# Kernel tuning notes

Measured on AMD Instinct MI355X. Metric: run time of the kernel, lower is better.

## Reference

```python
import jax, jax.numpy as jnp
import numpy as np
from jax import lax

STRIDES = (8, 16, 32, 64, 128)
LEVEL_HW = ((100, 128), (50, 64), (25, 32), (13, 16), (7, 8))
NUM_CLASSES = 80
PRE_NMS_THRESH = 0.05
PRE_NMS_TOPK = 1000
NMS_THRESH = 0.6
MAX_DET = 100
CLS_OFFSET = 1.0e4  # > max image coordinate, separates classes for joint NMS


def setup_inputs() -> dict:
    key = jax.random.key(0)
    B = 16
    ks = jax.random.split(key, 3 * len(LEVEL_HW))
    inp = {}
    i = 0
    for lvl, (h, w) in enumerate(LEVEL_HW):
        # shift logits down so sigmoid scores are mostly below the 0.05 candidate
        # threshold (realistic detection sparsity)
        inp[f"logits_p{lvl + 3}"] = jax.random.normal(ks[i], (B, NUM_CLASSES, h, w), jnp.float32) - 4.0; i += 1
        inp[f"bbox_p{lvl + 3}"] = jax.random.uniform(ks[i], (B, 4, h, w), jnp.float32, minval=0.0, maxval=64.0); i += 1
        inp[f"ctr_p{lvl + 3}"] = jax.random.normal(ks[i], (B, 1, h, w), jnp.float32); i += 1
    inp["im_info"] = jnp.tile(jnp.array([[800.0, 1024.0]], jnp.float32), (B, 1))
    return inp


def _locations(h, w, stride):
    # FCOSLocation: center of each stride cell -> [HW, 2] as (x, y)
    sx = jnp.arange(w, dtype=jnp.float32) * stride + stride // 2
    sy = jnp.arange(h, dtype=jnp.float32) * stride + stride // 2
    yy, xx = jnp.meshgrid(sy, sx, indexing="ij")
    return jnp.stack([xx.reshape(-1), yy.reshape(-1)], axis=-1)


def _nms_single(boxes, scores, classes):
    # boxes [K,4], scores [K] (descending), classes [K] int
    off = classes.astype(jnp.float32)[:, None] * CLS_OFFSET
    nb = boxes + off  # class-offset trick -> per-class NMS in one pass
    areas = jnp.maximum(nb[:, 2] - nb[:, 0], 0.0) * jnp.maximum(nb[:, 3] - nb[:, 1], 0.0)

    def body(sc, _):
        i = jnp.argmax(sc)
        s = sc[i]
        bi = nb[i]
        xx1 = jnp.maximum(bi[0], nb[:, 0])
        yy1 = jnp.maximum(bi[1], nb[:, 1])
        xx2 = jnp.minimum(bi[2], nb[:, 2])
        yy2 = jnp.minimum(bi[3], nb[:, 3])
        inter = jnp.maximum(xx2 - xx1, 0.0) * jnp.maximum(yy2 - yy1, 0.0)
        iou = inter / (areas[i] + areas - inter + 1e-9)
        sc2 = jnp.where(iou >= NMS_THRESH, -jnp.inf, sc).at[i].set(-jnp.inf)
        return sc2, (i, s > 0.0)

    _, (idxs, valid) = lax.scan(body, scores, None, length=MAX_DET)
    det = jnp.concatenate(
        [boxes[idxs], scores[idxs][:, None], classes[idxs].astype(jnp.float32)[:, None]],
        axis=-1,
    )  # [MAX_DET, 6] = x1,y1,x2,y2,score,class
    return jnp.where(valid[:, None], det, 0.0)


def _forward(logits_p3, bbox_p3, ctr_p3, logits_p4, bbox_p4, ctr_p4,
             logits_p5, bbox_p5, ctr_p5, logits_p6, bbox_p6, ctr_p6,
             logits_p7, bbox_p7, ctr_p7, im_info):
    levels = [(logits_p3, bbox_p3, ctr_p3), (logits_p4, bbox_p4, ctr_p4),
              (logits_p5, bbox_p5, ctr_p5), (logits_p6, bbox_p6, ctr_p6),
              (logits_p7, bbox_p7, ctr_p7)]
    scores_l, boxes_l = [], []
    for (lg, rg, ct), stride in zip(levels, STRIDES):
        B, C, H, W = lg.shape
        cls = jax.nn.sigmoid(lg).transpose(0, 2, 3, 1).reshape(B, H * W, C)
        cen = jax.nn.sigmoid(ct).transpose(0, 2, 3, 1).reshape(B, H * W, 1)
        # candidate threshold on raw class prob, then modulate by centerness
        comb = jnp.where(cls > PRE_NMS_THRESH, cls * cen, 0.0)
        locs = _locations(H, W, stride)  # [HW, 2]
        reg = rg.transpose(0, 2, 3, 1).reshape(B, H * W, 4)  # (l, t, r, b)
        bx = jnp.stack([locs[None, :, 0] - reg[..., 0],
                        locs[None, :, 1] - reg[..., 1],
                        locs[None, :, 0] + reg[..., 2],
                        locs[None, :, 1] + reg[..., 3]], axis=-1)
        scores_l.append(comb)
        boxes_l.append(bx)
    scores = jnp.concatenate(scores_l, axis=1)  # [B, N, C]
    boxes = jnp.concatenate(boxes_l, axis=1)    # [B, N, 4]
    B, N, C = scores.shape
    vals, idx = lax.top_k(scores.reshape(B, N * C), PRE_NMS_TOPK)  # [B, K]
    loc = idx // C
    cls_id = idx % C
    cand = jnp.take_along_axis(boxes, loc[..., None], axis=1)  # [B, K, 4]
    h = im_info[:, 0:1]
    w = im_info[:, 1:2]
    x1 = jnp.clip(cand[..., 0], 0.0, w - 1.0)
    y1 = jnp.clip(cand[..., 1], 0.0, h - 1.0)
    x2 = jnp.clip(cand[..., 2], 0.0, w - 1.0)
    y2 = jnp.clip(cand[..., 3], 0.0, h - 1.0)
    cand = jnp.stack([x1, y1, x2, y2], axis=-1)
    sc = jnp.where(vals > 0.0, jnp.sqrt(jnp.maximum(vals, 0.0) + 1e-12), 0.0)
    return jax.vmap(_nms_single)(cand, sc, cls_id)  # [B, MAX_DET, 6]


def reference(logits_p3, bbox_p3, ctr_p3, logits_p4, bbox_p4, ctr_p4,
              logits_p5, bbox_p5, ctr_p5, logits_p6, bbox_p6, ctr_p6,
              logits_p7, bbox_p7, ctr_p7, im_info):
    return _forward(logits_p3, bbox_p3, ctr_p3, logits_p4, bbox_p4, ctr_p4,
                    logits_p5, bbox_p5, ctr_p5, logits_p6, bbox_p6, ctr_p6,
                    logits_p7, bbox_p7, ctr_p7, im_info)
```

## Files before the change

### kernel.cpp

```cpp
#include <hip/hip_runtime.h>
#include <math.h>

#pragma clang fp contract(off)

#define NB 16
#define NC 80
#define NTOT 17064
#define TOPK 1000
#define NBINS 8192
#define CAP 4096
#define MAXDET 100
#define NREP 4
#define CNTSTRIDE 64
#define CHUNK 128
#define G1 128
#define NSEG 512
#define SEGW 1024

struct Ptrs {
    const float* lg[5];
    const float* bb[5];
    const float* ct[5];
};

__device__ __forceinline__ void level_of(int n, int& l, int& hw, int& W,
                                         int& stride, int& half, int& HW) {
    if (n < 12800)      { l = 0; hw = n;         W = 128; stride = 8;   half = 4;  HW = 12800; }
    else if (n < 16000) { l = 1; hw = n - 12800; W = 64;  stride = 16;  half = 8;  HW = 3200;  }
    else if (n < 16800) { l = 2; hw = n - 16000; W = 32;  stride = 32;  half = 16; HW = 800;   }
    else if (n < 17008) { l = 3; hw = n - 16800; W = 16;  stride = 64;  half = 32; HW = 208;   }
    else                { l = 4; hw = n - 17008; W = 8;   stride = 128; half = 64; HW = 56;    }
}

__device__ __forceinline__ float fast_sig(float x) {
    float e = __expf(-x);
    return __builtin_amdgcn_rcpf(1.0f + e);
}

template<int HW4, int NF4, int LVOFF, bool WRITE>
__device__ __forceinline__ void sweep_level(const float* lgb, const float* ctb,
        int tid, int lane, int bx, int gx, unsigned* lh32,
        unsigned long long* segp, unsigned& cur, unsigned long long ltmask) {
    for (int i0 = bx * 256; i0 < NF4; i0 += gx * 256) {
        int i = i0 + tid;
        bool f0 = false, f1 = false, f2 = false, f3 = false;
        unsigned long long k0 = 0, k1 = 0, k2 = 0, k3 = 0;
        if (i < NF4) {
            int c   = i / HW4;
            int hwf = i - c * HW4;
            float4 v  = *(const float4*)(lgb + c * (HW4 * 4) + hwf * 4);
            if (v.x > -2.95f || v.y > -2.95f || v.z > -2.95f || v.w > -2.95f) {
                float4 cv = *(const float4*)(ctb + hwf * 4);
                int nbase = LVOFF + hwf * 4;
#define DO_J(J, X, CT, F, K)                                                  \
                if ((X) > -2.95f) {                \
                    float cls = fast_sig(X);                                  \
                    if (cls > 0.04999f) {                                     \
                        bool in = true;                                       \
                        if (cls < 0.05001f)      \
                            in = (1.0f / (1.0f + expf(-(X)))) > 0.05f;        \
                        if (in) {                                             \
                            float cen = fast_sig(CT);                         \
                            float comb = cls * cen;                           \
                            unsigned bits = __float_as_uint(comb);            \
                            unsigned cb = (bits > 32u) ? bits - 32u : 0u;     \
                            unsigned bin = cb >> 19;                          \
                            atomicAdd(&lh32[bin >> 1],                        \
                                      (bin & 1u) ? 0x10000u : 1u);            \
                            if (WRITE) {                                      \
                                unsigned idx = (unsigned)((nbase + (J)) * NC + c);\
                                K = ((unsigned long long)bits << 32) |        \
                                    (0xFFFFFFFFu - idx);                      \
                                F = true;                                     \
                            }                                                 \
                        }                                                     \
                    }                                                         \
                }
                DO_J(0, v.x, cv.x, f0, k0)
                DO_J(1, v.y, cv.y, f1, k1)
                DO_J(2, v.z, cv.z, f2, k2)
                DO_J(3, v.w, cv.w, f3, k3)
#undef DO_J
            }
        }
        if (WRITE) {
            unsigned long long m0 = __ballot(f0), m1 = __ballot(f1);
            unsigned long long m2 = __ballot(f2), m3 = __ballot(f3);
            if ((m0 | m1 | m2 | m3) == 0ULL) continue;
            unsigned t0 = (unsigned)__popcll(m0), t1 = (unsigned)__popcll(m1);
            unsigned t2 = (unsigned)__popcll(m2), t3 = (unsigned)__popcll(m3);
            if (f0) { unsigned pos = cur + (unsigned)__popcll(m0 & ltmask);                if (pos < SEGW) segp[pos] = k0; }
            if (f1) { unsigned pos = cur + t0 + (unsigned)__popcll(m1 & ltmask);           if (pos < SEGW) segp[pos] = k1; }
            if (f2) { unsigned pos = cur + t0 + t1 + (unsigned)__popcll(m2 & ltmask);      if (pos < SEGW) segp[pos] = k2; }
            if (f3) { unsigned pos = cur + t0 + t1 + t2 + (unsigned)__popcll(m3 & ltmask); if (pos < SEGW) segp[pos] = k3; }
            cur += t0 + t1 + t2 + t3;
        }
    }
}

template<bool WRITE>
__global__ void __launch_bounds__(256) k_score1(Ptrs p, unsigned* hist,
                                                unsigned* segcnt,
                                                unsigned long long* segbuf) {
    __shared__ unsigned lh32[NBINS / 2];
    int b = blockIdx.y, tid = threadIdx.x, bx = blockIdx.x, gx = gridDim.x;
    int lane = tid & 63, wv = tid >> 6;
    unsigned long long ltmask = (1ULL << lane) - 1ULL;
    for (int i = tid; i < NBINS / 2; i += 256) lh32[i] = 0;
    __syncthreads();

    unsigned long long* segp = WRITE
        ? segbuf + (((size_t)b * G1 + bx) * 4 + wv) * SEGW : nullptr;
    unsigned cur = 0;

    sweep_level<3200, 256000,     0, WRITE>(p.lg[0] + (size_t)b * NC * 12800, p.ct[0] + (size_t)b * 12800, tid, lane, bx, gx, lh32, segp, cur, ltmask);
    sweep_level< 800,  64000, 12800, WRITE>(p.lg[1] + (size_t)b * NC * 3200,  p.ct[1] + (size_t)b * 3200,  tid, lane, bx, gx, lh32, segp, cur, ltmask);
    sweep_level< 200,  16000, 16000, WRITE>(p.lg[2] + (size_t)b * NC * 800,   p.ct[2] + (size_t)b * 800,   tid, lane, bx, gx, lh32, segp, cur, ltmask);
    sweep_level<  52,   4160, 16800, WRITE>(p.lg[3] + (size_t)b * NC * 208,   p.ct[3] + (size_t)b * 208,   tid, lane, bx, gx, lh32, segp, cur, ltmask);
    sweep_level<  14,   1120, 17008, WRITE>(p.lg[4] + (size_t)b * NC * 56,    p.ct[4] + (size_t)b * 56,    tid, lane, bx, gx, lh32, segp, cur, ltmask);

    if (WRITE && lane == 0)
        segcnt[(size_t)b * NSEG + bx * 4 + wv] = (cur < SEGW) ? cur : SEGW;

    __syncthreads();
    unsigned* h = hist + ((size_t)(bx & (NREP - 1)) * NB + b) * NBINS;
    for (int i = tid; i < NBINS; i += 256) {
        unsigned v = (lh32[i >> 1] >> ((i & 1) * 16)) & 0xFFFFu;
        if (v) atomicAdd(&h[i], v);
    }
}

__global__ void __launch_bounds__(256) k_thresh(const unsigned* hist, unsigned* T) {
    __shared__ unsigned hl[NBINS];
    __shared__ unsigned wtot[4];
    __shared__ int Tf;
    int b = blockIdx.x, tid = threadIdx.x, lane = tid & 63, wv = tid >> 6;
    if (tid == 0) Tf = 0;
    for (int i = tid; i < NBINS; i += 256) {
        unsigned s = 0;
        for (int r = 0; r < NREP; ++r)
            s += hist[((size_t)r * NB + b) * NBINS + i];
        hl[i] = s;
    }
    __syncthreads();
    int base = tid * 32;
    unsigned mysum = 0;
#pragma unroll
    for (int i = 0; i < 32; ++i) mysum += hl[base + i];
    unsigned incl = mysum;
#pragma unroll
    for (int off = 1; off < 64; off <<= 1) {
        unsigned v = __shfl_down(incl, off);
        if (lane + off < 64) incl += v;
    }
    if (lane == 0) wtot[wv] = incl;
    __syncthreads();
    unsigned above = 0;
    for (int w = wv + 1; w < 4; ++w) above += wtot[w];
    unsigned sufincl = incl + above;
    unsigned excl = sufincl - mysum;
    if (excl < TOPK && sufincl >= TOPK) {
        unsigned running = excl;
        for (int bin = base + 31; bin >= base; --bin) {
            running += hl[bin];
            if (running >= TOPK) { Tf = bin; break; }
        }
    }
    __syncthreads();
    if (tid == 0) T[b] = (unsigned)Tf;
}

__global__ void __launch_bounds__(256) k_filter(Ptrs p, const unsigned* T,
                                                const unsigned* segcnt,
                                                const unsigned long long* segbuf,
                                                unsigned* cnt2, unsigned long long* sel) {
    int b = blockIdx.y, tid = threadIdx.x, lane = tid & 63;
    unsigned Tb = T[b];
    unsigned Tshift = Tb << 19;
    unsigned fmin = (Tshift >= 32u) ? Tshift - 32u : 0u;
    unsigned long long ltmask = (1ULL << lane) - 1ULL;
    unsigned* cntb = cnt2 + (size_t)b * CNTSTRIDE;
    unsigned long long* selb = sel + (size_t)b * CAP;

    for (int sg = blockIdx.x * 16; sg < blockIdx.x * 16 + 16; ++sg) {
        unsigned sc = segcnt[(size_t)b * NSEG + sg];
        const unsigned long long* src = segbuf + ((size_t)b * NSEG + sg) * SEGW;
        for (int i = tid; i < (int)sc; i += 256) {
            unsigned long long e = src[i];
            bool f = false;
            unsigned long long key = 0;
            if ((unsigned)(e >> 32) >= fmin) {
                unsigned idx = 0xFFFFFFFFu - (unsigned)(e & 0xFFFFFFFFu);
                int n = idx / NC, c = idx - n * NC;
                int l, hw, W, stride, half, HW;
                level_of(n, l, hw, W, stride, half, HW);
                float x  = p.lg[l][(size_t)b * NC * HW + (size_t)c * HW + hw];
                float ct = p.ct[l][(size_t)b * HW + hw];
                float cls = 1.0f / (1.0f + expf(-x));
                float cen = 1.0f / (1.0f + expf(-ct));
                unsigned be = __float_as_uint(cls * cen);
                if ((be >> 19) >= Tb) {
                    key = ((unsigned long long)be << 32) | (e & 0xFFFFFFFFULL);
                    f = true;
                }
            }
            unsigned long long mk = __ballot(f);
            if (mk) {
                unsigned nw = (unsigned)__popcll(mk);
                int basep = 0;
                if (lane == 0) basep = (int)atomicAdd(cntb, nw);
                basep = __shfl(basep, 0);
                if (f) {
                    int pos = basep + (int)__popcll(mk & ltmask);
                    if (pos < CAP) selb[pos] = key;
                }
            }
        }
    }
}

template<int HW4, int NF4, int LVOFF>
__device__ __forceinline__ void compact_level(const float* lgb, const float* ctb,
        int tid, int lane, int bx, int gx, unsigned Tb, float xpre,
        unsigned* cntb, unsigned long long* selb, unsigned long long ltmask) {
    for (int i0 = bx * 256; i0 < NF4; i0 += gx * 256) {
        int i = i0 + tid;
        bool f0 = false, f1 = false, f2 = false, f3 = false;
        unsigned long long k0 = 0, k1 = 0, k2 = 0, k3 = 0;
        if (i < NF4) {
            int c   = i / HW4;
            int hwf = i - c * HW4;
            float4 v = *(const float4*)(lgb + c * (HW4 * 4) + hwf * 4);
            if (v.x > xpre || v.y > xpre || v.z > xpre || v.w > xpre) {
                float4 cv = *(const float4*)(ctb + hwf * 4);
                int nbase = LVOFF + hwf * 4;
#define DO_J(J, X, CT, F, K)                                                  \
                if ((X) > xpre) {                                             \
                    float cls = 1.0f / (1.0f + expf(-(X)));                   \
                    if (cls > 0.05f) {                                        \
                        float cen = 1.0f / (1.0f + expf(-(CT)));              \
                        float comb = cls * cen;                               \
                        unsigned bits = __float_as_uint(comb);                \
                        if ((bits >> 19) >= Tb) {                             \
                            unsigned idx = (unsigned)((nbase + (J)) * NC + c);\
                            K = ((unsigned long long)bits << 32) |            \
                                (0xFFFFFFFFu - idx);                          \
                            F = true;                                         \
                        }                                                     \
                    }                                                         \
                }
                DO_J(0, v.x, cv.x, f0, k0)
                DO_J(1, v.y, cv.y, f1, k1)
                DO_J(2, v.z, cv.z, f2, k2)
                DO_J(3, v.w, cv.w, f3, k3)
#undef DO_J
            }
        }
        unsigned long long m0 = __ballot(f0), m1 = __ballot(f1);
        unsigned long long m2 = __ballot(f2), m3 = __ballot(f3);
        if ((m0 | m1 | m2 | m3) == 0ULL) continue;
        unsigned t0 = (unsigned)__popcll(m0), t1 = (unsigned)__popcll(m1);
        unsigned t2 = (unsigned)__popcll(m2), t3 = (unsigned)__popcll(m3);
        unsigned total = t0 + t1 + t2 + t3;
        int basep = 0;
        if (lane == 0) basep = (int)atomicAdd(cntb, total);
        basep = __shfl(basep, 0);
        if (f0) { int pos = basep + (int)__popcll(m0 & ltmask);                       if (pos < CAP) selb[pos] = k0; }
        if (f1) { int pos = basep + (int)t0 + (int)__popcll(m1 & ltmask);             if (pos < CAP) selb[pos] = k1; }
        if (f2) { int pos = basep + (int)(t0 + t1) + (int)__popcll(m2 & ltmask);      if (pos < CAP) selb[pos] = k2; }
        if (f3) { int pos = basep + (int)(t0 + t1 + t2) + (int)__popcll(m3 & ltmask); if (pos < CAP) selb[pos] = k3; }
    }
}

__global__ void __launch_bounds__(256) k_compactB(Ptrs p, const unsigned* T,
                                                  unsigned* cnt2, unsigned long long* sel) {
    int b = blockIdx.y, tid = threadIdx.x, lane = tid & 63;
    int bx = blockIdx.x, gx = gridDim.x;
    unsigned Tb = T[b];
    float mthr = __uint_as_float(Tb << 19);
    float xpre = -2.95f;
    if (mthr > 1e-37f && mthr < 1.0f) {
        float lm = logf(mthr / (1.0f - mthr)) - 0.01f;
        if (lm > xpre) xpre = lm;
    }
    unsigned long long ltmask = (1ULL << lane) - 1ULL;
    unsigned* cntb = cnt2 + (size_t)b * CNTSTRIDE;
    unsigned long long* selb = sel + (size_t)b * CAP;
    compact_level<3200, 256000,     0>(p.lg[0] + (size_t)b * NC * 12800, p.ct[0] + (size_t)b * 12800, tid, lane, bx, gx, Tb, xpre, cntb, selb, ltmask);
    compact_level< 800,  64000, 12800>(p.lg[1] + (size_t)b * NC * 3200,  p.ct[1] + (size_t)b * 3200,  tid, lane, bx, gx, Tb, xpre, cntb, selb, ltmask);
    compact_level< 200,  16000, 16000>(p.lg[2] + (size_t)b * NC * 800,   p.ct[2] + (size_t)b * 800,   tid, lane, bx, gx, Tb, xpre, cntb, selb, ltmask);
    compact_level<  52,   4160, 16800>(p.lg[3] + (size_t)b * NC * 208,   p.ct[3] + (size_t)b * 208,   tid, lane, bx, gx, Tb, xpre, cntb, selb, ltmask);
    compact_level<  14,   1120, 17008>(p.lg[4] + (size_t)b * NC * 56,    p.ct[4] + (size_t)b * 56,    tid, lane, bx, gx, Tb, xpre, cntb, selb, ltmask);
}

__global__ void __launch_bounds__(256) k_rankdec(Ptrs p, const unsigned* cnt,
                                                 const unsigned long long* sel,
                                                 const float* im_info, float* cand) {
    __shared__ __align__(16) unsigned long long keys[CAP];
    int b = blockIdx.y, tid = threadIdx.x;
    unsigned M = cnt[(size_t)b * CNTSTRIDE];
    if (M > CAP) M = CAP;
    int s0 = blockIdx.x * 256;
    if (s0 >= (int)M) return;
    int Mpad = (int)((M + 1u) & ~1u);
    for (int i = tid; i < Mpad; i += 256)
        keys[i] = (i < (int)M) ? sel[(size_t)b * CAP + i] : 0ULL;
    __syncthreads();

    int s = s0 + tid;
    if (s >= (int)M) return;
    unsigned long long k = keys[s];
    int rank = 0;
    for (int j = 0; j < Mpad; j += 2) {
        ulonglong2 kk = *(const ulonglong2*)&keys[j];
        rank += (kk.x > k) ? 1 : 0;
        rank += (kk.y > k) ? 1 : 0;
    }
    if (rank >= TOPK) return;

    float Him = im_info[b * 2 + 0], Wim = im_info[b * 2 + 1];
    float xmax = Wim - 1.0f, ymax = Him - 1.0f;
    unsigned sb = (unsigned)(k >> 32);
    unsigned idx = 0xFFFFFFFFu - (unsigned)(k & 0xFFFFFFFFu);
    float val = __uint_as_float(sb);
    int n = idx / NC, c = idx - n * NC;
    int l, hw, W, stride, half, HW;
    level_of(n, l, hw, W, stride, half, HW);
    int wx = hw % W, hy = hw / W;
    float locx = (float)(wx * stride + half);
    float locy = (float)(hy * stride + half);
    const float* bb = p.bb[l] + (size_t)b * 4 * HW + hw;
    float r0 = bb[0], r1 = bb[(size_t)HW], r2 = bb[(size_t)2 * HW], r3 = bb[(size_t)3 * HW];
    float x1 = locx - r0, y1 = locy - r1, x2 = locx + r2, y2 = locy + r3;
    x1 = fminf(fmaxf(x1, 0.f), xmax);
    y1 = fminf(fmaxf(y1, 0.f), ymax);
    x2 = fminf(fmaxf(x2, 0.f), xmax);
    y2 = fminf(fmaxf(y2, 0.f), ymax);
    float scv = sqrtf(val + 1e-12f);
    float off = (float)c * 10000.0f;
    float a0 = x1 + off, a1 = y1 + off, a2 = x2 + off, a3 = y2 + off;
    float area = fmaxf(a2 - a0, 0.f) * fmaxf(a3 - a1, 0.f);
    float* dst = cand + ((size_t)b * TOPK + rank) * 12;
    *(float4*)(dst + 0) = make_float4(x1, y1, x2, y2);
    *(float4*)(dst + 4) = make_float4(a0, a1, a2, a3);
    *(float4*)(dst + 8) = make_float4(area, scv, (float)c, 0.f);
}

__global__ void __launch_bounds__(64) k_nms(const unsigned* cnt, const float* cand,
                                            float* out) {
    __shared__ float4 s_ob[CHUNK], s_nb[CHUNK], s_ms[CHUNK];
    int b = blockIdx.x, lane = threadIdx.x;
    unsigned M = cnt[(size_t)b * CNTSTRIDE];
    if (M > CAP) M = CAP;
    int ncand = (int)M < TOPK ? (int)M : TOPK;
    const float* src = cand + (size_t)b * TOPK * 12;
    float* ob = out + (size_t)b * MAXDET * 6;

    int na = 0;
    float4 a0b = make_float4(0.f, 0.f, 0.f, 0.f);
    float4 a1b = make_float4(0.f, 0.f, 0.f, 0.f);
    float a0a = 0.f, a1a = 0.f;

    for (int base = 0; base < ncand && na < MAXDET; base += CHUNK) {
        int cn = ncand - base; if (cn > CHUNK) cn = CHUNK;
        for (int cidx = lane; cidx < cn; cidx += 64) {
            const float* s = src + (size_t)(base + cidx) * 12;
            s_ob[cidx] = *(const float4*)(s + 0);
            s_nb[cidx] = *(const float4*)(s + 4);
            s_ms[cidx] = *(const float4*)(s + 8);
        }
        __syncthreads();
        for (int r = 0; r < cn && na < MAXDET; ++r) {
            float4 cb = s_nb[r];
            float ca = s_ms[r].x;
            bool sup = false;
            if (lane < na) {
                float xx1 = fmaxf(a0b.x, cb.x);
                float yy1 = fmaxf(a0b.y, cb.y);
                float xx2 = fminf(a0b.z, cb.z);
                float yy2 = fminf(a0b.w, cb.w);
                float inter = fmaxf(xx2 - xx1, 0.f) * fmaxf(yy2 - yy1, 0.f);
                float iou = inter / (((a0a + ca) - inter) + 1e-9f);
                sup = (iou >= 0.6f);
            }
            if (lane + 64 < na) {
                float xx1 = fmaxf(a1b.x, cb.x);
                float yy1 = fmaxf(a1b.y, cb.y);
                float xx2 = fminf(a1b.z, cb.z);
                float yy2 = fminf(a1b.w, cb.w);
                float inter = fmaxf(xx2 - xx1, 0.f) * fmaxf(yy2 - yy1, 0.f);
                float iou = inter / (((a1a + ca) - inter) + 1e-9f);
                sup |= (iou >= 0.6f);
            }
            if (__ballot(sup) == 0ULL) {
                if (lane == (na & 63)) {
                    if (na < 64) { a0b = cb; a0a = ca; }
                    else         { a1b = cb; a1a = ca; }
                }
                if (lane == 0) {
                    float4 o4 = s_ob[r]; float4 m4 = s_ms[r];
                    ob[na * 6 + 0] = o4.x; ob[na * 6 + 1] = o4.y;
                    ob[na * 6 + 2] = o4.z; ob[na * 6 + 3] = o4.w;
                    ob[na * 6 + 4] = m4.y; ob[na * 6 + 5] = m4.z;
                }
                ++na;
            }
        }
        __syncthreads();
    }
    for (int q = na * 6 + lane; q < MAXDET * 6; q += 64)
        ob[q] = 0.f;
}

extern "C" void kernel_launch(void* const* d_in, const int* in_sizes, int n_in,
                              void* d_out, int out_size, void* d_ws, size_t ws_size,
                              hipStream_t stream) {
    Ptrs p;
    for (int l = 0; l < 5; ++l) {
        p.lg[l] = (const float*)d_in[3 * l + 0];
        p.bb[l] = (const float*)d_in[3 * l + 1];
        p.ct[l] = (const float*)d_in[3 * l + 2];
    }
    const float* im_info = (const float*)d_in[15];
    float* out = (float*)d_out;

    unsigned char* w = (unsigned char*)d_ws;
    unsigned* hist          = (unsigned*)(w);
    unsigned* cnt2          = (unsigned*)(w + 2097152);
    unsigned* T             = (unsigned*)(w + 2101248);
    unsigned long long* sel = (unsigned long long*)(w + 2101504);
    float* cand             = (float*)(w + 2625792);
    unsigned* segcnt        = (unsigned*)(w + 3393792);
    unsigned long long* segbuf = (unsigned long long*)(w + 3426560);
    const bool big = ws_size >= (size_t)70535424;

    hipMemsetAsync(w, 0, 2101504, stream);

    if (big) {
        k_score1<true ><<<dim3(G1, NB), 256, 0, stream>>>(p, hist, segcnt, segbuf);
        k_thresh<<<NB, 256, 0, stream>>>(hist, T);
        k_filter<<<dim3(NSEG / 16, NB), 256, 0, stream>>>(p, T, segcnt, segbuf, cnt2, sel);
    } else {
        k_score1<false><<<dim3(G1, NB), 256, 0, stream>>>(p, hist, nullptr, nullptr);
        k_thresh<<<NB, 256, 0, stream>>>(hist, T);
        k_compactB<<<dim3(128, NB), 256, 0, stream>>>(p, T, cnt2, sel);
    }
    k_rankdec<<<dim3(16, NB), 256, 0, stream>>>(p, cnt2, sel, im_info, cand);
    k_nms<<<NB, 64, 0, stream>>>(cnt2, cand, out);
}
```

Baseline: 257.2 us.

## Prefilter candidates at fixed score floor and build histogram from compacted segments

```diff
diff --git a/kernel.cpp b/kernel.cpp
--- a/kernel.cpp
+++ b/kernel.cpp
@@ -15,7 +15,7 @@
 #define CHUNK 128
 #define G1 128
 #define NSEG 512
-#define SEGW 1024
+#define SEGW 512
 
 struct Ptrs {
     const float* lg[5];
@@ -37,9 +37,9 @@
     return __builtin_amdgcn_rcpf(1.0f + e);
 }
 
-template<int HW4, int NF4, int LVOFF, bool WRITE>
-__device__ __forceinline__ void sweep_level(const float* lgb, const float* ctb,
-        int tid, int lane, int bx, int gx, unsigned* lh32,
+template<int HW4, int NF4, int LVOFF>
+__device__ __forceinline__ void scan_level(const float* lgb, const float* ctb,
+        int tid, int lane, int bx, int gx, unsigned FB_LO,
         unsigned long long* segp, unsigned& cur, unsigned long long ltmask) {
     for (int i0 = bx * 256; i0 < NF4; i0 += gx * 256) {
         int i = i0 + tid;
@@ -48,32 +48,20 @@
         if (i < NF4) {
             int c   = i / HW4;
             int hwf = i - c * HW4;
-            float4 v  = *(const float4*)(lgb + c * (HW4 * 4) + hwf * 4);
-            if (v.x > -2.95f || v.y > -2.95f || v.z > -2.95f || v.w > -2.95f) {
+            float4 v = *(const float4*)(lgb + c * (HW4 * 4) + hwf * 4);
+            if (v.x > -2.47f || v.y > -2.47f || v.z > -2.47f || v.w > -2.47f) {
                 float4 cv = *(const float4*)(ctb + hwf * 4);
                 int nbase = LVOFF + hwf * 4;
 #define DO_J(J, X, CT, F, K)                                                  \
-                if ((X) > -2.95f) {                \
+                if ((X) > -2.47f) {                                           \
                     float cls = fast_sig(X);                                  \
-                    if (cls > 0.04999f) {                                     \
-                        bool in = true;                                       \
-                        if (cls < 0.05001f)      \
-                            in = (1.0f / (1.0f + expf(-(X)))) > 0.05f;        \
-                        if (in) {                                             \
-                            float cen = fast_sig(CT);                         \
-                            float comb = cls * cen;                           \
-                            unsigned bits = __float_as_uint(comb);            \
-                            unsigned cb = (bits > 32u) ? bits - 32u : 0u;     \
-                            unsigned bin = cb >> 19;                          \
-                            atomicAdd(&lh32[bin >> 1],                        \
-                                      (bin & 1u) ? 0x10000u : 1u);            \
-                            if (WRITE) {                                      \
-                                unsigned idx = (unsigned)((nbase + (J)) * NC + c);\
-                                K = ((unsigned long long)bits << 32) |        \
-                                    (0xFFFFFFFFu - idx);                      \
-                                F = true;                                     \
-                            }                                                 \
-                        }                                                     \
+                    float cen = fast_sig(CT);                                 \
+                    unsigned bits = __float_as_uint(cls * cen);               \
+                    if (bits >= FB_LO) {                                      \
+                        unsigned idx = (unsigned)((nbase + (J)) * NC + c);    \
+                        K = ((unsigned long long)bits << 32) |                \
+                            (0xFFFFFFFFu - idx);                              \
+                        F = true;                                             \
                     }                                                         \
                 }
                 DO_J(0, v.x, cv.x, f0, k0)
@@ -83,70 +71,131 @@
 #undef DO_J
             }
         }
-        if (WRITE) {
-            unsigned long long m0 = __ballot(f0), m1 = __ballot(f1);
-            unsigned long long m2 = __ballot(f2), m3 = __ballot(f3);
-            if ((m0 | m1 | m2 | m3) == 0ULL) continue;
-            unsigned t0 = (unsigned)__popcll(m0), t1 = (unsigned)__popcll(m1);
-            unsigned t2 = (unsigned)__popcll(m2), t3 = (unsigned)__popcll(m3);
-            if (f0) { unsigned pos = cur + (unsigned)__popcll(m0 & ltmask);                if (pos < SEGW) segp[pos] = k0; }
-            if (f1) { unsigned pos = cur + t0 + (unsigned)__popcll(m1 & ltmask);           if (pos < SEGW) segp[pos] = k1; }
-            if (f2) { unsigned pos = cur + t0 + t1 + (unsigned)__popcll(m2 & ltmask);      if (pos < SEGW) segp[pos] = k2; }
-            if (f3) { unsigned pos = cur + t0 + t1 + t2 + (unsigned)__popcll(m3 & ltmask); if (pos < SEGW) segp[pos] = k3; }
-            cur += t0 + t1 + t2 + t3;
-        }
-    }
-}
-
-template<bool WRITE>
-__global__ void __launch_bounds__(256) k_score1(Ptrs p, unsigned* hist,
-                                                unsigned* segcnt,
-                                                unsigned long long* segbuf) {
-    __shared__ unsigned lh32[NBINS / 2];
+        unsigned long long m0 = __ballot(f0), m1 = __ballot(f1);
+        unsigned long long m2 = __ballot(f2), m3 = __ballot(f3);
+        if ((m0 | m1 | m2 | m3) == 0ULL) continue;
+        unsigned t0 = (unsigned)__popcll(m0), t1 = (unsigned)__popcll(m1);
+        unsigned t2 = (unsigned)__popcll(m2), t3 = (unsigned)__popcll(m3);
+        if (f0) { unsigned pos = cur + (unsigned)__popcll(m0 & ltmask);                if (pos < SEGW) segp[pos] = k0; }
+        if (f1) { unsigned pos = cur + t0 + (unsigned)__popcll(m1 & ltmask);           if (pos < SEGW) segp[pos] = k1; }
+        if (f2) { unsigned pos = cur + t0 + t1 + (unsigned)__popcll(m2 & ltmask);      if (pos < SEGW) segp[pos] = k2; }
+        if (f3) { unsigned pos = cur + t0 + t1 + t2 + (unsigned)__popcll(m3 & ltmask); if (pos < SEGW) segp[pos] = k3; }
+        cur += t0 + t1 + t2 + t3;
+    }
+}
+
+__global__ void __launch_bounds__(256) k_scoreF(Ptrs p, unsigned* segcnt,
+                                                unsigned long long* segbuf,
+                                                unsigned* cnt2) {
     int b = blockIdx.y, tid = threadIdx.x, bx = blockIdx.x, gx = gridDim.x;
     int lane = tid & 63, wv = tid >> 6;
+    if (bx == 0 && tid == 0) cnt2[(size_t)b * CNTSTRIDE] = 0;
     unsigned long long ltmask = (1ULL << lane) - 1ULL;
-    for (int i = tid; i < NBINS / 2; i += 256) lh32[i] = 0;
-    __syncthreads();
-
-    unsigned long long* segp = WRITE
-        ? segbuf + (((size_t)b * G1 + bx) * 4 + wv) * SEGW : nullptr;
+    unsigned FB_LO = __float_as_uint(0.08f) - 64u;
+    unsigned long long* segp = segbuf + (((size_t)b * G1 + bx) * 4 + wv) * SEGW;
     unsigned cur = 0;
 
-    sweep_level<3200, 256000,     0, WRITE>(p.lg[0] + (size_t)b * NC * 12800, p.ct[0] + (size_t)b * 12800, tid, lane, bx, gx, lh32, segp, cur, ltmask);
-    sweep_level< 800,  64000, 12800, WRITE>(p.lg[1] + (size_t)b * NC * 3200,  p.ct[1] + (size_t)b * 3200,  tid, lane, bx, gx, lh32, segp, cur, ltmask);
-    sweep_level< 200,  16000, 16000, WRITE>(p.lg[2] + (size_t)b * NC * 800,   p.ct[2] + (size_t)b * 800,   tid, lane, bx, gx, lh32, segp, cur, ltmask);
-    sweep_level<  52,   4160, 16800, WRITE>(p.lg[3] + (size_t)b * NC * 208,   p.ct[3] + (size_t)b * 208,   tid, lane, bx, gx, lh32, segp, cur, ltmask);
-    sweep_level<  14,   1120, 17008, WRITE>(p.lg[4] + (size_t)b * NC * 56,    p.ct[4] + (size_t)b * 56,    tid, lane, bx, gx, lh32, segp, cur, ltmask);
-
-    if (WRITE && lane == 0)
-        segcnt[(size_t)b * NSEG + bx * 4 + wv] = (cur < SEGW) ? cur : SEGW;
-
-    __syncthreads();
-    unsigned* h = hist + ((size_t)(bx & (NREP - 1)) * NB + b) * NBINS;
-    for (int i = tid; i < NBINS; i += 256) {
-        unsigned v = (lh32[i >> 1] >> ((i & 1) * 16)) & 0xFFFFu;
-        if (v) atomicAdd(&h[i], v);
-    }
-}
-
-__global__ void __launch_bounds__(256) k_thresh(const unsigned* hist, unsigned* T) {
-    __shared__ unsigned hl[NBINS];
-    __shared__ unsigned wtot[4];
+    scan_level<3200, 256000,     0>(p.lg[0] + (size_t)b * NC * 12800, p.ct[0] + (size_t)b * 12800, tid, lane, bx, gx, FB_LO, segp, cur, ltmask);
+    scan_level< 800,  64000, 12800>(p.lg[1] + (size_t)b * NC * 3200,  p.ct[1] + (size_t)b * 3200,  tid, lane, bx, gx, FB_LO, segp, cur, ltmask);
+    scan_level< 200,  16000, 16000>(p.lg[2] + (size_t)b * NC * 800,   p.ct[2] + (size_t)b * 800,   tid, lane, bx, gx, FB_LO, segp, cur, ltmask);
+    scan_level<  52,   4160, 16800>(p.lg[3] + (size_t)b * NC * 208,   p.ct[3] + (size_t)b * 208,   tid, lane, bx, gx, FB_LO, segp, cur, ltmask);
+    scan_level<  14,   1120, 17008>(p.lg[4] + (size_t)b * NC * 56,    p.ct[4] + (size_t)b * 56,    tid, lane, bx, gx, FB_LO, segp, cur, ltmask);
+
+    if (lane == 0) segcnt[(size_t)b * NSEG + bx * 4 + wv] = cur;
+}
+
+template<int HW4, int NF4>
+__device__ __forceinline__ void histf_level(const float* lgb, const float* ctb,
+                                            int tid, unsigned* hist) {
+    for (int i0 = 0; i0 < NF4; i0 += 1024) {
+        int i = i0 + tid;
+        if (i < NF4) {
+            int c   = i / HW4;
+            int hwf = i - c * HW4;
+            float4 v = *(const float4*)(lgb + c * (HW4 * 4) + hwf * 4);
+            if (v.x > -2.95f || v.y > -2.95f || v.z > -2.95f || v.w > -2.95f) {
+                float4 cv = *(const float4*)(ctb + hwf * 4);
+                float xs[4] = {v.x, v.y, v.z, v.w};
+                float cs[4] = {cv.x, cv.y, cv.z, cv.w};
+#pragma unroll
+                for (int j = 0; j < 4; ++j) {
+                    float x = xs[j];
+                    if (x > -2.95f) {
+                        float cls = fast_sig(x);
+                        if (cls > 0.04999f) {
+                            bool in = true;
+                            if (cls < 0.05001f)
+                                in = (1.0f / (1.0f + expf(-x))) > 0.05f;
+                            if (in) {
+                                float cen = fast_sig(cs[j]);
+                                unsigned bits = __float_as_uint(cls * cen);
+                                unsigned cb = (bits > 32u) ? bits - 32u : 0u;
+                                atomicAdd(&hist[cb >> 19], 1u);
+                            }
+                        }
+                    }
+                }
+            }
+        }
+    }
+}
+
+__global__ void __launch_bounds__(1024) k_threshF(Ptrs p, const unsigned* segcnt,
+                                                  const unsigned long long* segbuf,
+                                                  unsigned* T, unsigned* okf) {
+    __shared__ unsigned hist[NBINS];
+    __shared__ unsigned wred[16], wtot[16];
+    __shared__ int s_flags;
     __shared__ int Tf;
     int b = blockIdx.x, tid = threadIdx.x, lane = tid & 63, wv = tid >> 6;
-    if (tid == 0) Tf = 0;
-    for (int i = tid; i < NBINS; i += 256) {
-        unsigned s = 0;
-        for (int r = 0; r < NREP; ++r)
-            s += hist[((size_t)r * NB + b) * NBINS + i];
-        hl[i] = s;
-    }
-    __syncthreads();
-    int base = tid * 32;
+    if (tid == 0) { s_flags = 0; Tf = 0; }
+    for (int i = tid; i < NBINS; i += 1024) hist[i] = 0;
+    __syncthreads();
+
+    bool ovf = false;
+    for (int sg = wv; sg < NSEG; sg += 16) {
+        unsigned cnt = segcnt[(size_t)b * NSEG + sg];
+        if (cnt > SEGW) { ovf = true; cnt = SEGW; }
+        const unsigned long long* src = segbuf + ((size_t)b * NSEG + sg) * SEGW;
+        for (int i = lane; i < (int)cnt; i += 64) {
+            unsigned bits = (unsigned)(src[i] >> 32);
+            unsigned cb = (bits > 32u) ? bits - 32u : 0u;
+            atomicAdd(&hist[cb >> 19], 1u);
+        }
+    }
+    if (ovf) atomicOr(&s_flags, 1);
+    __syncthreads();
+
+    const unsigned B0 = __float_as_uint(0.08f);
+    const int OKBIN = (int)(B0 >> 19) + 1;
+    int base = tid * 8;
+    unsigned okp = 0;
+#pragma unroll
+    for (int i = 0; i < 8; ++i) if (base + i >= OKBIN) okp += hist[base + i];
+    for (int off = 32; off > 0; off >>= 1) okp += __shfl_down(okp, off);
+    if (lane == 0) wred[wv] = okp;
+    __syncthreads();
+    if (tid == 0) {
+        unsigned tot = 0;
+        for (int w = 0; w < 16; ++w) tot += wred[w];
+        if ((s_flags & 1) || tot < TOPK) atomicOr(&s_flags, 2);
+    }
+    __syncthreads();
+
+    if (s_flags & 2) {
+        for (int i = tid; i < NBINS; i += 1024) hist[i] = 0;
+        __syncthreads();
+        histf_level<3200, 256000>(p.lg[0] + (size_t)b * NC * 12800, p.ct[0] + (size_t)b * 12800, tid, hist);
+        histf_level< 800,  64000>(p.lg[1] + (size_t)b * NC * 3200,  p.ct[1] + (size_t)b * 3200,  tid, hist);
+        histf_level< 200,  16000>(p.lg[2] + (size_t)b * NC * 800,   p.ct[2] + (size_t)b * 800,   tid, hist);
+        histf_level<  52,   4160>(p.lg[3] + (size_t)b * NC * 208,   p.ct[3] + (size_t)b * 208,   tid, hist);
+        histf_level<  14,   1120>(p.lg[4] + (size_t)b * NC * 56,    p.ct[4] + (size_t)b * 56,    tid, hist);
+        __syncthreads();
+    }
+
     unsigned mysum = 0;
 #pragma unroll
-    for (int i = 0; i < 32; ++i) mysum += hl[base + i];
+    for (int i = 0; i < 8; ++i) mysum += hist[base + i];
     unsigned incl = mysum;
 #pragma unroll
     for (int off = 1; off < 64; off <<= 1) {
@@ -156,67 +205,18 @@
     if (lane == 0) wtot[wv] = incl;
     __syncthreads();
     unsigned above = 0;
-    for (int w = wv + 1; w < 4; ++w) above += wtot[w];
+    for (int w = wv + 1; w < 16; ++w) above += wtot[w];
     unsigned sufincl = incl + above;
     unsigned excl = sufincl - mysum;
     if (excl < TOPK && sufincl >= TOPK) {
         unsigned running = excl;
-        for (int bin = base + 31; bin >= base; --bin) {
-            running += hl[bin];
+        for (int bin = base + 7; bin >= base; --bin) {
+            running += hist[bin];
             if (running >= TOPK) { Tf = bin; break; }
         }
     }
     __syncthreads();
-    if (tid == 0) T[b] = (unsigned)Tf;
-}
-
-__global__ void __launch_bounds__(256) k_filter(Ptrs p, const unsigned* T,
-                                                const unsigned* segcnt,
-                                                const unsigned long long* segbuf,
-                                                unsigned* cnt2, unsigned long long* sel) {
-    int b = blockIdx.y, tid = threadIdx.x, lane = tid & 63;
-    unsigned Tb = T[b];
-    unsigned Tshift = Tb << 19;
-    unsigned fmin = (Tshift >= 32u) ? Tshift - 32u : 0u;
-    unsigned long long ltmask = (1ULL << lane) - 1ULL;
-    unsigned* cntb = cnt2 + (size_t)b * CNTSTRIDE;
-    unsigned long long* selb = sel + (size_t)b * CAP;
-
-    for (int sg = blockIdx.x * 16; sg < blockIdx.x * 16 + 16; ++sg) {
-        unsigned sc = segcnt[(size_t)b * NSEG + sg];
-        const unsigned long long* src = segbuf + ((size_t)b * NSEG + sg) * SEGW;
-        for (int i = tid; i < (int)sc; i += 256) {
-            unsigned long long e = src[i];
-            bool f = false;
-            unsigned long long key = 0;
-            if ((unsigned)(e >> 32) >= fmin) {
-                unsigned idx = 0xFFFFFFFFu - (unsigned)(e & 0xFFFFFFFFu);
-                int n = idx / NC, c = idx - n * NC;
-                int l, hw, W, stride, half, HW;
-                level_of(n, l, hw, W, stride, half, HW);
-                float x  = p.lg[l][(size_t)b * NC * HW + (size_t)c * HW + hw];
-                float ct = p.ct[l][(size_t)b * HW + hw];
-                float cls = 1.0f / (1.0f + expf(-x));
-                float cen = 1.0f / (1.0f + expf(-ct));
-                unsigned be = __float_as_uint(cls * cen);
-                if ((be >> 19) >= Tb) {
-                    key = ((unsigned long long)be << 32) | (e & 0xFFFFFFFFULL);
-                    f = true;
-                }
-            }
-            unsigned long long mk = __ballot(f);
-            if (mk) {
-                unsigned nw = (unsigned)__popcll(mk);
-                int basep = 0;
-                if (lane == 0) basep = (int)atomicAdd(cntb, nw);
-                basep = __shfl(basep, 0);
-                if (f) {
-                    int pos = basep + (int)__popcll(mk & ltmask);
-                    if (pos < CAP) selb[pos] = key;
-                }
-            }
-        }
-    }
+    if (tid == 0) { T[b] = (unsigned)Tf; okf[b] = (s_flags & 2) ? 0u : 1u; }
 }
 
 template<int HW4, int NF4, int LVOFF>
@@ -272,6 +272,169 @@
     }
 }
 
+__global__ void __launch_bounds__(256) k_filterF(Ptrs p, const unsigned* T,
+                                                 const unsigned* okf,
+                                                 const unsigned* segcnt,
+                                                 const unsigned long long* segbuf,
+                                                 unsigned* cnt2, unsigned long long* sel) {
+    int b = blockIdx.y, tid = threadIdx.x, lane = tid & 63;
+    int bx = blockIdx.x, gx = gridDim.x;
+    unsigned Tb = T[b];
+    unsigned long long ltmask = (1ULL << lane) - 1ULL;
+    unsigned* cntb = cnt2 + (size_t)b * CNTSTRIDE;
+    unsigned long long* selb = sel + (size_t)b * CAP;
+
+    if (okf[b]) {
+        unsigned Tshift = Tb << 19;
+        unsigned fmin = (Tshift >= 32u) ? Tshift - 32u : 0u;
+        int per = NSEG / gx;
+        for (int sg = bx * per; sg < bx * per + per; ++sg) {
+            unsigned sc = segcnt[(size_t)b * NSEG + sg];
+            if (sc > SEGW) sc = SEGW;
+            const unsigned long long* src = segbuf + ((size_t)b * NSEG + sg) * SEGW;
+            for (int i = tid; i < (int)sc; i += 256) {
+                unsigned long long e = src[i];
+                bool f = false;
+                unsigned long long key = 0;
+                if ((unsigned)(e >> 32) >= fmin) {
+                    unsigned idx = 0xFFFFFFFFu - (unsigned)(e & 0xFFFFFFFFu);
+                    int n = idx / NC, c = idx - n * NC;
+                    int l, hw, W, stride, half, HW;
+                    level_of(n, l, hw, W, stride, half, HW);
+                    float x  = p.lg[l][(size_t)b * NC * HW + (size_t)c * HW + hw];
+                    float ct = p.ct[l][(size_t)b * HW + hw];
+                    float cls = 1.0f / (1.0f + expf(-x));
+                    if (cls > 0.05f) {
+                        float cen = 1.0f / (1.0f + expf(-ct));
+                        unsigned be = __float_as_uint(cls * cen);
+                        if ((be >> 19) >= Tb) {
+                            key = ((unsigned long long)be << 32) | (e & 0xFFFFFFFFULL);
+                            f = true;
+                        }
+                    }
+                }
+                unsigned long long mk = __ballot(f);
+                if (mk) {
+                    unsigned nw = (unsigned)__popcll(mk);
+                    int basep = 0;
+                    if (lane == 0) basep = (int)atomicAdd(cntb, nw);
+                    basep = __shfl(basep, 0);
+                    if (f) {
+                        int pos = basep + (int)__popcll(mk & ltmask);
+                        if (pos < CAP) selb[pos] = key;
+                    }
+                }
+            }
+        }
+    } else {
+        float mthr = __uint_as_float(Tb << 19);
+        float xpre = -2.95f;
+        if (mthr > 1e-37f && mthr < 1.0f) {
+            float lm = logf(mthr / (1.0f - mthr)) - 0.01f;
+            if (lm > xpre) xpre = lm;
+        }
+        compact_level<3200, 256000,     0>(p.lg[0] + (size_t)b * NC * 12800, p.ct[0] + (size_t)b * 12800, tid, lane, bx, gx, Tb, xpre, cntb, selb, ltmask);
+        compact_level< 800,  64000, 12800>(p.lg[1] + (size_t)b * NC * 3200,  p.ct[1] + (size_t)b * 3200,  tid, lane, bx, gx, Tb, xpre, cntb, selb, ltmask);
+        compact_level< 200,  16000, 16000>(p.lg[2] + (size_t)b * NC * 800,   p.ct[2] + (size_t)b * 800,   tid, lane, bx, gx, Tb, xpre, cntb, selb, ltmask);
+        compact_level<  52,   4160, 16800>(p.lg[3] + (size_t)b * NC * 208,   p.ct[3] + (size_t)b * 208,   tid, lane, bx, gx, Tb, xpre, cntb, selb, ltmask);
+        compact_level<  14,   1120, 17008>(p.lg[4] + (size_t)b * NC * 56,    p.ct[4] + (size_t)b * 56,    tid, lane, bx, gx, Tb, xpre, cntb, selb, ltmask);
+    }
+}
+
+template<int HW4, int NF4>
+__device__ __forceinline__ void hist_level(const float* lgb, const float* ctb,
+                                           int tid, int bx, int gx, unsigned* lh) {
+    for (int i0 = bx * 256; i0 < NF4; i0 += gx * 256) {
+        int i = i0 + tid;
+        if (i < NF4) {
+            int c   = i / HW4;
+            int hwf = i - c * HW4;
+            float4 v  = *(const float4*)(lgb + c * (HW4 * 4) + hwf * 4);
+            if (v.x > -2.95f || v.y > -2.95f || v.z > -2.95f || v.w > -2.95f) {
+                float4 cv = *(const float4*)(ctb + hwf * 4);
+                float xs[4] = {v.x, v.y, v.z, v.w};
+                float cs[4] = {cv.x, cv.y, cv.z, cv.w};
+#pragma unroll
+                for (int j = 0; j < 4; ++j) {
+                    float x = xs[j];
+                    if (x > -2.95f) {
+                        float cls = fast_sig(x);
+                        if (cls > 0.04999f) {
+                            bool in = true;
+                            if (cls < 0.05001f)
+                                in = (1.0f / (1.0f + expf(-x))) > 0.05f;
+                            if (in) {
+                                float cen = fast_sig(cs[j]);
+                                unsigned bits = __float_as_uint(cls * cen);
+                                unsigned cb = (bits > 32u) ? bits - 32u : 0u;
+                                atomicAdd(&lh[cb >> 19], 1u);
+                            }
+                        }
+                    }
+                }
+            }
+        }
+    }
+}
+
+__global__ void __launch_bounds__(256) k_histA(Ptrs p, unsigned* hist) {
+    __shared__ unsigned lh[NBINS];
+    int b = blockIdx.y, tid = threadIdx.x, bx = blockIdx.x, gx = gridDim.x;
+    for (int i = tid; i < NBINS; i += 256) lh[i] = 0;
+    __syncthreads();
+    hist_level<3200, 256000>(p.lg[0] + (size_t)b * NC * 12800, p.ct[0] + (size_t)b * 12800, tid, bx, gx, lh);
+    hist_level< 800,  64000>(p.lg[1] + (size_t)b * NC * 3200,  p.ct[1] + (size_t)b * 3200,  tid, bx, gx, lh);
+    hist_level< 200,  16000>(p.lg[2] + (size_t)b * NC * 800,   p.ct[2] + (size_t)b * 800,   tid, bx, gx, lh);
+    hist_level<  52,   4160>(p.lg[3] + (size_t)b * NC * 208,   p.ct[3] + (size_t)b * 208,   tid, bx, gx, lh);
+    hist_level<  14,   1120>(p.lg[4] + (size_t)b * NC * 56,    p.ct[4] + (size_t)b * 56,    tid, bx, gx, lh);
+    __syncthreads();
+    unsigned* h = hist + ((size_t)(bx & (NREP - 1)) * NB + b) * NBINS;
+    for (int i = tid; i < NBINS; i += 256) {
+        unsigned v = lh[i];
+        if (v) atomicAdd(&h[i], v);
+    }
+}
+
+__global__ void __launch_bounds__(256) k_thresh(const unsigned* hist, unsigned* T) {
+    __shared__ unsigned hl[NBINS];
+    __shared__ unsigned wtot[4];
+    __shared__ int Tf;
+    int b = blockIdx.x, tid = threadIdx.x, lane = tid & 63, wv = tid >> 6;
+    if (tid == 0) Tf = 0;
+    for (int i = tid; i < NBINS; i += 256) {
+        unsigned s = 0;
+        for (int r = 0; r < NREP; ++r)
+            s += hist[((size_t)r * NB + b) * NBINS + i];
+        hl[i] = s;
+    }
+    __syncthreads();
+    int base = tid * 32;
+    unsigned mysum = 0;
+#pragma unroll
+    for (int i = 0; i < 32; ++i) mysum += hl[base + i];
+    unsigned incl = mysum;
+#pragma unroll
+    for (int off = 1; off < 64; off <<= 1) {
+        unsigned v = __shfl_down(incl, off);
+        if (lane + off < 64) incl += v;
+    }
+    if (lane == 0) wtot[wv] = incl;
+    __syncthreads();
+    unsigned above = 0;
+    for (int w = wv + 1; w < 4; ++w) above += wtot[w];
+    unsigned sufincl = incl + above;
+    unsigned excl = sufincl - mysum;
+    if (excl < TOPK && sufincl >= TOPK) {
+        unsigned running = excl;
+        for (int bin = base + 31; bin >= base; --bin) {
+            running += hl[bin];
+            if (running >= TOPK) { Tf = bin; break; }
+        }
+    }
+    __syncthreads();
+    if (tid == 0) T[b] = (unsigned)Tf;
+}
+
 __global__ void __launch_bounds__(256) k_compactB(Ptrs p, const unsigned* T,
                                                   unsigned* cnt2, unsigned long long* sel) {
     int b = blockIdx.y, tid = threadIdx.x, lane = tid & 63;
@@ -423,28 +586,34 @@
     }
     const float* im_info = (const float*)d_in[15];
     float* out = (float*)d_out;
-
     unsigned char* w = (unsigned char*)d_ws;
-    unsigned* hist          = (unsigned*)(w);
-    unsigned* cnt2          = (unsigned*)(w + 2097152);
-    unsigned* T             = (unsigned*)(w + 2101248);
-    unsigned long long* sel = (unsigned long long*)(w + 2101504);
-    float* cand             = (float*)(w + 2625792);
-    unsigned* segcnt        = (unsigned*)(w + 3393792);
-    unsigned long long* segbuf = (unsigned long long*)(w + 3426560);
-    const bool big = ws_size >= (size_t)70535424;
-
-    hipMemsetAsync(w, 0, 2101504, stream);
-
-    if (big) {
-        k_score1<true ><<<dim3(G1, NB), 256, 0, stream>>>(p, hist, segcnt, segbuf);
-        k_thresh<<<NB, 256, 0, stream>>>(hist, T);
-        k_filter<<<dim3(NSEG / 16, NB), 256, 0, stream>>>(p, T, segcnt, segbuf, cnt2, sel);
+
+    if (ws_size >= (size_t)34884096) {
+        unsigned* segcnt           = (unsigned*)(w);
+        unsigned* cnt2             = (unsigned*)(w + 32768);
+        unsigned* T                = (unsigned*)(w + 36864);
+        unsigned* okf              = (unsigned*)(w + 37120);
+        unsigned long long* sel    = (unsigned long long*)(w + 37376);
+        float* cand                = (float*)(w + 561664);
+        unsigned long long* segbuf = (unsigned long long*)(w + 1329664);
+
+        k_scoreF<<<dim3(G1, NB), 256, 0, stream>>>(p, segcnt, segbuf, cnt2);
+        k_threshF<<<NB, 1024, 0, stream>>>(p, segcnt, segbuf, T, okf);
+        k_filterF<<<dim3(32, NB), 256, 0, stream>>>(p, T, okf, segcnt, segbuf, cnt2, sel);
+        k_rankdec<<<dim3(16, NB), 256, 0, stream>>>(p, cnt2, sel, im_info, cand);
+        k_nms<<<NB, 64, 0, stream>>>(cnt2, cand, out);
     } else {
-        k_score1<false><<<dim3(G1, NB), 256, 0, stream>>>(p, hist, nullptr, nullptr);
+        unsigned* hist          = (unsigned*)(w);
+        unsigned* cnt2          = (unsigned*)(w + 2097152);
+        unsigned* T             = (unsigned*)(w + 2101248);
+        unsigned long long* sel = (unsigned long long*)(w + 2101504);
+        float* cand             = (float*)(w + 2625792);
+
+        hipMemsetAsync(w, 0, 2101504, stream);
+        k_histA<<<dim3(64, NB), 256, 0, stream>>>(p, hist);
         k_thresh<<<NB, 256, 0, stream>>>(hist, T);
         k_compactB<<<dim3(128, NB), 256, 0, stream>>>(p, T, cnt2, sel);
-    }
-    k_rankdec<<<dim3(16, NB), 256, 0, stream>>>(p, cnt2, sel, im_info, cand);
-    k_nms<<<NB, 64, 0, stream>>>(cnt2, cand, out);
-}
+        k_rankdec<<<dim3(16, NB), 256, 0, stream>>>(p, cnt2, sel, im_info, cand);
+        k_nms<<<NB, 64, 0, stream>>>(cnt2, cand, out);
+    }
+}
```

After: 277.1 us. +7.7%, slower.
